# Kernel optimization log

Hardware: AMD Instinct MI355X
Metric: run time of the kernel (lower is better)

Reference implementation:

```python
import jax, jax.numpy as jnp
import numpy as np

H, D = 8, 16
HD = H * D
SCALE0 = float(1.0 / np.sqrt(D * 1))   # degree-0 dot-product scale (order m=1)
SCALE1 = float(1.0 / np.sqrt(D * 3))   # degree-1 dot-product scale (order m=3)
SHARED = float(np.sqrt(0.5))           # shared_scale = sqrt(1/2) for DOT_PROD + SHARED
NEG = -1e9


def _split_heads_q(x):  # (b,n,HD,m) -> (b,H,n,D,m)
    b, n, _, m = x.shape
    return x.reshape(b, n, H, D, m).transpose(0, 2, 1, 3, 4)


def _split_heads_k(x):  # (b,n,N,HD,m) -> (b,H,n,N,D,m)
    b, n, N, _, m = x.shape
    return x.reshape(b, n, N, H, D, m).transpose(0, 3, 1, 2, 4, 5)


def _augment_kv(k, v, feats, W_self, null_k, null_v):
    # attend_self: VNLinear self key/value; use_null_kv: learned null tokens.
    b, n = feats.shape[:2]
    m = feats.shape[-1]
    skv = jnp.einsum('oc,bncm->bnom', W_self, feats)          # (b,n,2HD,m)
    sk, sv = jnp.split(skv, 2, axis=-2)
    sk = _split_heads_q(sk)[:, :, :, None]                     # (b,H,n,1,D,m)
    sv = _split_heads_q(sv)[:, :, :, None]
    nk = jnp.broadcast_to(null_k[None, :, None, None], (b, H, n, 1, D, m))
    nv = jnp.broadcast_to(null_v[None, :, None, None], (b, H, n, 1, D, m))
    k = jnp.concatenate([nk, sk, k], axis=3)                   # (b,H,n,2+N,D,m)
    v = jnp.concatenate([nv, sv, v], axis=3)
    return k, v


def _merge_heads(x):  # (b,H,n,D,m) -> (b,n,HD,m)
    b, _, n, _, m = x.shape
    return x.transpose(0, 2, 1, 3, 4).reshape(b, n, HD, m)


def _forward(q0, k0, v0, q1, k1, v1, feats0, feats1, edges,
             W_self_kv0, W_self_kv1, W_bias, self_bias, null_bias,
             null_k0, null_v0, null_k1, null_v1, head_weights1,
             W_out0, W_out1, neighbor_mask):
    b, n, N = edges.shape[:3]
    q0h, k0h, v0h = _split_heads_q(q0), _split_heads_k(k0), _split_heads_k(v0)
    q1h, k1h, v1h = _split_heads_q(q1), _split_heads_k(k1), _split_heads_k(v1)
    k0h, v0h = _augment_kv(k0h, v0h, feats0, W_self_kv0, null_k0, null_v0)
    k1h, v1h = _augment_kv(k1h, v1h, feats1, W_self_kv1, null_k1, null_v1)

    # pair bias for degree 0 (to_order==1); prepend null/self bias columns
    edge_bias = jnp.einsum('bnje,he->bhnj', edges, W_bias)     # (b,H,n,N)
    nb = jnp.broadcast_to(null_bias[None, :, None, None], (b, H, n, 1))
    sb = jnp.broadcast_to(self_bias[None, :, None, None], (b, H, n, 1))
    bias = jnp.concatenate([nb, sb, edge_bias], axis=-1)        # (b,H,n,2+N)

    sim0 = jnp.einsum('bhndm,bhnjdm->bhnj', q0h, k0h) * SCALE0 + bias
    w1 = jax.nn.softplus(head_weights1)                         # (1,H,1,1)
    sim1 = jnp.einsum('bhndm,bhnjdm->bhnj', q1h, k1h) * (SCALE1 * w1)

    total = (sim0 + sim1) * SHARED
    mask = jnp.concatenate(
        [jnp.ones((b, 1, n, 2), dtype=bool),                    # null + self always valid
         neighbor_mask[:, None]], axis=-1)
    total = jnp.where(mask, total, NEG)
    attn = jax.nn.softmax(total, axis=-1)                       # shared across degrees

    out0 = _merge_heads(jnp.einsum('bhnj,bhnjdm->bhndm', attn, v0h))
    out1 = _merge_heads(jnp.einsum('bhnj,bhnjdm->bhndm', attn, v1h))

    y0 = jnp.einsum('oc,bncm->bnom', W_out0, out0)              # FiberLinear deg 0
    y1 = jnp.einsum('oc,bncm->bnom', W_out1, out1)              # FiberLinear deg 1
    return y0, y1


def setup_inputs() -> dict:
    key = jax.random.key(0)
    ks = jax.random.split(key, 20)
    b, n, N, e = 1, 2048, 32, 32
    d0, d1 = 128, 64
    f = lambda k, s: jax.random.normal(k, s, dtype=jnp.float32) * 0.1
    return {
        'q0': f(ks[0], (b, n, HD, 1)), 'k0': f(ks[1], (b, n, N, HD, 1)), 'v0': f(ks[2], (b, n, N, HD, 1)),
        'q1': f(ks[3], (b, n, HD, 3)), 'k1': f(ks[4], (b, n, N, HD, 3)), 'v1': f(ks[5], (b, n, N, HD, 3)),
        'feats0': f(ks[6], (b, n, d0, 1)), 'feats1': f(ks[7], (b, n, d1, 3)),
        'edges': f(ks[8], (b, n, N, e)),
        'W_self_kv0': f(ks[9], (2 * HD, d0)), 'W_self_kv1': f(ks[10], (2 * HD, d1)),
        'W_bias': f(ks[11], (H, e)),
        'self_bias': jnp.zeros((H,), jnp.float32), 'null_bias': jnp.zeros((H,), jnp.float32),
        'null_k0': jnp.zeros((H, D, 1), jnp.float32), 'null_v0': jnp.zeros((H, D, 1), jnp.float32),
        'null_k1': jnp.zeros((H, D, 3), jnp.float32), 'null_v1': jnp.zeros((H, D, 3), jnp.float32),
        'head_weights1': jnp.full((1, H, 1, 1), float(np.log(np.e - 1.0)), jnp.float32),
        'W_out0': f(ks[12], (d0, HD)), 'W_out1': f(ks[13], (d1, HD)),
        'neighbor_mask': jax.random.uniform(ks[14], (b, n, N)) > 0.1,
    }


def reference(q0, k0, v0, q1, k1, v1, feats0, feats1, edges,
              W_self_kv0, W_self_kv1, W_bias, self_bias, null_bias,
              null_k0, null_v0, null_k1, null_v1, head_weights1,
              W_out0, W_out1, neighbor_mask):
    return _forward(q0, k0, v0, q1, k1, v1, feats0, feats1, edges,
                    W_self_kv0, W_self_kv1, W_bias, self_bias, null_bias,
                    null_k0, null_v0, null_k1, null_v1, head_weights1,
                    W_out0, W_out1, neighbor_mask)
```

## Files before the change

kernel.cpp:

```cpp
#include <hip/hip_runtime.h>

constexpr int kH  = 8;
constexpr int kD  = 16;
constexpr int kHD = 128;
constexpr int kN  = 32;
constexpr int kE  = 32;
constexpr int kD0 = 128;
constexpr int kD1 = 64;
constexpr int kP  = 4;
constexpr int kP3 = 2;
constexpr int kPP = 8;

constexpr float SCALE0   = 0.25f;
constexpr float SCALE1   = 0.14433756729740643f;
constexpr float SHARED_S = 0.70710678118654752f;
constexpr float NEGV     = -1e9f;


__global__ __launch_bounds__(256) void k1_selfkv(
    const float* __restrict__ q0, const float* __restrict__ q1,
    const float* __restrict__ feats0, const float* __restrict__ feats1,
    const float* __restrict__ Wskv0, const float* __restrict__ Wskv1,
    const float* __restrict__ self_bias, const float* __restrict__ null_bias,
    const float* __restrict__ nk0, const float* __restrict__ nk1,
    const float* __restrict__ hw1,
    float* __restrict__ ws_sc, float* __restrict__ ws_sv0, float* __restrict__ ws_sv1)
{
  const int i0 = blockIdx.x * kP;
  const int t  = threadIdx.x;
  __shared__ __align__(16) float f0s[kP][kD0];
  __shared__ __align__(16) float f1s[kP][kD1 * 3];
  __shared__ __align__(16) float q0s[kP][kHD];
  __shared__ __align__(16) float q1s[kP][kHD * 3];
  __shared__ float sk0L[kP][kHD];
  __shared__ float sk1L[kP][kHD * 3];
  __shared__ float w1s[kH];

  for (int u = t; u < kP * 32; u += 256) { int p = u >> 5, r = u & 31;
    ((float4*)f0s[p])[r] = ((const float4*)(feats0 + (size_t)(i0 + p) * kD0))[r]; }
  for (int u = t; u < kP * 48; u += 256) { int p = u / 48, r = u % 48;
    ((float4*)f1s[p])[r] = ((const float4*)(feats1 + (size_t)(i0 + p) * kD1 * 3))[r]; }
  for (int u = t; u < kP * 32; u += 256) { int p = u >> 5, r = u & 31;
    ((float4*)q0s[p])[r] = ((const float4*)(q0 + (size_t)(i0 + p) * kHD))[r]; }
  for (int u = t; u < kP * 96; u += 256) { int p = u / 96, r = u % 96;
    ((float4*)q1s[p])[r] = ((const float4*)(q1 + (size_t)(i0 + p) * kHD * 3))[r]; }
  if (t < kH) w1s[t] = log1pf(expf(hw1[t]));
  __syncthreads();

  float acc0[kP] = {};
  {
    const float4* wr = (const float4*)(Wskv0 + t * kD0);
    #pragma unroll
    for (int g = 0; g < 32; ++g) {
      float4 w = wr[g]; int c = g * 4;
      #pragma unroll
      for (int p = 0; p < kP; ++p)
        acc0[p] += w.x * f0s[p][c] + w.y * f0s[p][c + 1]
                 + w.z * f0s[p][c + 2] + w.w * f0s[p][c + 3];
    }
  }
  float acc1[kP][3] = {};
  {
    const float4* wr = (const float4*)(Wskv1 + t * kD1);
    #pragma unroll
    for (int g = 0; g < 16; ++g) {
      float4 w = wr[g]; int c = g * 4;
      float wv[4] = {w.x, w.y, w.z, w.w};
      #pragma unroll
      for (int q = 0; q < 4; ++q) {
        #pragma unroll
        for (int p = 0; p < kP; ++p) {
          const float* fp = &f1s[p][(c + q) * 3];
          acc1[p][0] += wv[q] * fp[0];
          acc1[p][1] += wv[q] * fp[1];
          acc1[p][2] += wv[q] * fp[2];
        }
      }
    }
  }
  if (t < kHD) {
    #pragma unroll
    for (int p = 0; p < kP; ++p) {
      sk0L[p][t] = acc0[p];
      sk1L[p][t * 3 + 0] = acc1[p][0];
      sk1L[p][t * 3 + 1] = acc1[p][1];
      sk1L[p][t * 3 + 2] = acc1[p][2];
    }
  } else {
    const int o = t - kHD;
    #pragma unroll
    for (int p = 0; p < kP; ++p) {
      ws_sv0[(size_t)(i0 + p) * kHD + o] = acc0[p];
      float* sp = ws_sv1 + (size_t)(i0 + p) * kHD * 3 + o * 3;
      sp[0] = acc1[p][0]; sp[1] = acc1[p][1]; sp[2] = acc1[p][2];
    }
  }
  __syncthreads();

  if (t < kP * 16) {
    const int p = t >> 4, idx = t & 15;
    const int h = idx & 7;
    const bool is_self = idx >= 8;
    float s0 = 0.f, s1 = 0.f, bias;
    if (is_self) {
      #pragma unroll
      for (int d = 0; d < kD; ++d) s0 += q0s[p][h * kD + d] * sk0L[p][h * kD + d];
      #pragma unroll
      for (int x = 0; x < 48; ++x) s1 += q1s[p][h * 48 + x] * sk1L[p][h * 48 + x];
      bias = self_bias[h];
    } else {
      #pragma unroll
      for (int d = 0; d < kD; ++d) s0 += q0s[p][h * kD + d] * nk0[h * kD + d];
      #pragma unroll
      for (int x = 0; x < 48; ++x) s1 += q1s[p][h * 48 + x] * nk1[h * 48 + x];
      bias = null_bias[h];
    }
    float total = (s0 * SCALE0 + bias + s1 * SCALE1 * w1s[h]) * SHARED_S;
    ws_sc[(size_t)(i0 + p) * 272 + h * 34 + (is_self ? 1 : 0)] = total;
  }
}

__global__ __launch_bounds__(256) void k2_sims(
    const float* __restrict__ q0, const float* __restrict__ q1,
    const float* __restrict__ k0, const float* __restrict__ k1,
    const float* __restrict__ edges, const float* __restrict__ Wbias,
    const float* __restrict__ hw1, const int* __restrict__ nmask,
    float* __restrict__ ws_sc)
{
  const int i0 = blockIdx.x * kP;
  const int t  = threadIdx.x;
  __shared__ float q0s[kP][kH * 17];
  __shared__ float q1s[kP][kH * 49];
  __shared__ float edg[kP][kN * 33];
  __shared__ float wbT[kE * kH];
  __shared__ float w1s[kH];
  __shared__ __align__(16) float scL[kP][272];

  for (int u = t; u < kP * 32; u += 256) { int p = u >> 5, r = u & 31;
    float4 v = ((const float4*)(q0 + (size_t)(i0 + p) * kHD))[r];
    int c = r * 4, h = c >> 4, d = c & 15;
    float* dst = &q0s[p][h * 17 + d];
    dst[0] = v.x; dst[1] = v.y; dst[2] = v.z; dst[3] = v.w; }
  for (int u = t; u < kP * 96; u += 256) { int p = u / 96, r = u % 96;
    float4 v = ((const float4*)(q1 + (size_t)(i0 + p) * kHD * 3))[r];
    int c = r * 4, h = c / 48, x = c % 48;
    float* dst = &q1s[p][h * 49 + x];
    dst[0] = v.x; dst[1] = v.y; dst[2] = v.z; dst[3] = v.w; }
  for (int u = t; u < kP * 256; u += 256) { int p = u >> 8, r = u & 255;
    float4 v = ((const float4*)(edges + (size_t)(i0 + p) * kN * kE))[r];
    int j = r >> 3, e4 = (r & 7) * 4;
    float* dst = &edg[p][j * 33 + e4];
    dst[0] = v.x; dst[1] = v.y; dst[2] = v.z; dst[3] = v.w; }
  if (t < kH * kE) { int h = t >> 5, e = t & 31; wbT[e * 8 + h] = Wbias[t]; }
  if (t < kH) w1s[t] = log1pf(expf(hw1[t]));
  if (t < kP * 16) { int p = t >> 4, idx = t & 15, h = idx & 7, slot = idx >> 3;
    scL[p][h * 34 + slot] = ws_sc[(size_t)(i0 + p) * 272 + h * 34 + slot]; }
  __syncthreads();

  {
    const int j = t >> 3, h = t & 7;
    #pragma unroll
    for (int p = 0; p < kP; ++p) {
      const int i = i0 + p;
      float bias = 0.f;
      #pragma unroll
      for (int e = 0; e < kE; ++e) bias += edg[p][j * 33 + e] * wbT[e * 8 + h];
      float s0 = 0.f;
      const float4* kr0 = (const float4*)(k0 + (size_t)(i * kN + j) * kHD + h * kD);
      #pragma unroll
      for (int g = 0; g < 4; ++g) {
        float4 w = kr0[g]; int x = h * 17 + g * 4;
        s0 += w.x * q0s[p][x] + w.y * q0s[p][x + 1]
            + w.z * q0s[p][x + 2] + w.w * q0s[p][x + 3];
      }
      float s1 = 0.f;
      const float4* kr1 = (const float4*)(k1 + (size_t)(i * kN + j) * kHD * 3 + h * 48);
      #pragma unroll
      for (int g = 0; g < 12; ++g) {
        float4 w = kr1[g]; int x = h * 49 + g * 4;
        s1 += w.x * q1s[p][x] + w.y * q1s[p][x + 1]
            + w.z * q1s[p][x + 2] + w.w * q1s[p][x + 3];
      }
      float total = (s0 * SCALE0 + bias + s1 * SCALE1 * w1s[h]) * SHARED_S;
      bool valid = nmask[(size_t)i * kN + j] != 0;
      scL[p][h * 34 + 2 + j] = valid ? total : NEGV;
    }
  }
  __syncthreads();

  if (t < kP * kH) {
    const int p = t >> 3, h = t & 7;
    float* row = &scL[p][h * 34];
    float mx = -1e30f;
    #pragma unroll
    for (int u = 0; u < 34; ++u) mx = fmaxf(mx, row[u]);
    float sum = 0.f;
    #pragma unroll
    for (int u = 0; u < 34; ++u) sum += __expf(row[u] - mx);
    float inv = 1.f / sum;
    #pragma unroll
    for (int u = 0; u < 34; ++u) row[u] = __expf(row[u] - mx) * inv;
  }
  __syncthreads();

  for (int u = t; u < kP * 68; u += 256) {
    int p = u / 68, r = u % 68;
    ((float4*)(ws_sc + (size_t)(i0 + p) * 272))[r] = ((float4*)scL[p])[r];
  }
}

__global__ __launch_bounds__(256, 4) void k3_accum(
    const float* __restrict__ v0, const float* __restrict__ v1,
    const float* __restrict__ nv0, const float* __restrict__ nv1,
    const float* __restrict__ ws_sc,
    float* __restrict__ ws_sv0, float* __restrict__ ws_sv1)
{
  const int i0 = blockIdx.x * kP3;
  const int t  = threadIdx.x;
  __shared__ __align__(16) float attnL[kP3][272];

  if (t < kP3 * 68) {
    int p = t / 68, r = t % 68;
    ((float4*)attnL[p])[r] = ((const float4*)(ws_sc + (size_t)(i0 + p) * 272))[r];
  }
  __syncthreads();

  const int p = t >> 7, i = i0 + p;
  const int s = t & 127;
  float4 acc;
  if (s < 32) {
    const int h = s >> 2;
    const float* at = attnL[p] + h * 34;
    float4 nv = ((const float4*)nv0)[s];
    float4 sv = ((const float4*)(ws_sv0 + (size_t)i * kHD))[s];
    acc.x = at[0] * nv.x + at[1] * sv.x;
    acc.y = at[0] * nv.y + at[1] * sv.y;
    acc.z = at[0] * nv.z + at[1] * sv.z;
    acc.w = at[0] * nv.w + at[1] * sv.w;
    const float4* vp = (const float4*)(v0 + (size_t)i * kN * kHD) + s;
    float4 vbuf[8];
    #pragma unroll
    for (int g = 0; g < 4; ++g) {
      #pragma unroll
      for (int r = 0; r < 8; ++r) vbuf[r] = vp[(g * 8 + r) * 32];
      #pragma unroll
      for (int r = 0; r < 8; ++r) {
        float a = at[2 + g * 8 + r];
        acc.x += a * vbuf[r].x; acc.y += a * vbuf[r].y;
        acc.z += a * vbuf[r].z; acc.w += a * vbuf[r].w;
      }
    }
    ((float4*)(ws_sv0 + (size_t)i * kHD))[s] = acc;
  } else {
    const int s1 = s - 32;
    const int h = s1 / 12;
    const float* at = attnL[p] + h * 34;
    float4 nv = ((const float4*)nv1)[s1];
    float4 sv = ((const float4*)(ws_sv1 + (size_t)i * kHD * 3))[s1];
    acc.x = at[0] * nv.x + at[1] * sv.x;
    acc.y = at[0] * nv.y + at[1] * sv.y;
    acc.z = at[0] * nv.z + at[1] * sv.z;
    acc.w = at[0] * nv.w + at[1] * sv.w;
    const float4* vp = (const float4*)(v1 + (size_t)i * kN * kHD * 3) + s1;
    float4 vbuf[8];
    #pragma unroll
    for (int g = 0; g < 4; ++g) {
      #pragma unroll
      for (int r = 0; r < 8; ++r) vbuf[r] = vp[(g * 8 + r) * 96];
      #pragma unroll
      for (int r = 0; r < 8; ++r) {
        float a = at[2 + g * 8 + r];
        acc.x += a * vbuf[r].x; acc.y += a * vbuf[r].y;
        acc.z += a * vbuf[r].z; acc.w += a * vbuf[r].w;
      }
    }
    ((float4*)(ws_sv1 + (size_t)i * kHD * 3))[s1] = acc;
  }
}

__global__ __launch_bounds__(320) void k4_proj(
    const float* __restrict__ ws_o0, const float* __restrict__ ws_o1,
    const float* __restrict__ Wout0, const float* __restrict__ Wout1,
    float* __restrict__ out, int n_total)
{
  const int i0 = blockIdx.x * kPP;
  const int t  = threadIdx.x;
  __shared__ __align__(16) float o0L[kPP][kHD];
  __shared__ __align__(16) float o1L[kPP][kHD * 3];

  for (int u = t; u < kPP * 32; u += 320) { int p = u >> 5, r = u & 31;
    ((float4*)o0L[p])[r] = ((const float4*)(ws_o0 + (size_t)(i0 + p) * kHD))[r]; }
  for (int u = t; u < kPP * 96; u += 320) { int p = u / 96, r = u % 96;
    ((float4*)o1L[p])[r] = ((const float4*)(ws_o1 + (size_t)(i0 + p) * kHD * 3))[r]; }
  __syncthreads();

  if (t < 128) {
    float acc[kPP] = {};
    const float4* wr = (const float4*)(Wout0 + t * kHD);
    #pragma unroll
    for (int g = 0; g < 32; ++g) {
      float4 w = wr[g]; int c = g * 4;
      #pragma unroll
      for (int p = 0; p < kPP; ++p)
        acc[p] += w.x * o0L[p][c] + w.y * o0L[p][c + 1]
                + w.z * o0L[p][c + 2] + w.w * o0L[p][c + 3];
    }
    #pragma unroll
    for (int p = 0; p < kPP; ++p) out[(size_t)(i0 + p) * kHD + t] = acc[p];
  } else {
    const int v2 = t - 128, o = v2 / 3, m = v2 - o * 3;
    float acc[kPP] = {};
    const float4* wr = (const float4*)(Wout1 + o * kHD);
    #pragma unroll
    for (int g = 0; g < 32; ++g) {
      float4 w = wr[g]; int c = g * 4;
      #pragma unroll
      for (int p = 0; p < kPP; ++p)
        acc[p] += w.x * o1L[p][(c + 0) * 3 + m] + w.y * o1L[p][(c + 1) * 3 + m]
                + w.z * o1L[p][(c + 2) * 3 + m] + w.w * o1L[p][(c + 3) * 3 + m];
    }
    #pragma unroll
    for (int p = 0; p < kPP; ++p)
      out[(size_t)n_total * kHD + (size_t)(i0 + p) * 192 + v2] = acc[p];
  }
}

extern "C" void kernel_launch(void* const* d_in, const int* in_sizes, int n_in,
                              void* d_out, int out_size, void* d_ws, size_t ws_size,
                              hipStream_t stream) {
  const int n = in_sizes[0] / kHD;
  const float* q0     = (const float*)d_in[0];
  const float* k0     = (const float*)d_in[1];
  const float* v0     = (const float*)d_in[2];
  const float* q1     = (const float*)d_in[3];
  const float* k1     = (const float*)d_in[4];
  const float* v1     = (const float*)d_in[5];
  const float* feats0 = (const float*)d_in[6];
  const float* feats1 = (const float*)d_in[7];
  const float* edges  = (const float*)d_in[8];
  const float* Wskv0  = (const float*)d_in[9];
  const float* Wskv1  = (const float*)d_in[10];
  const float* Wbias  = (const float*)d_in[11];
  const float* sbias  = (const float*)d_in[12];
  const float* nbias  = (const float*)d_in[13];
  const float* nk0    = (const float*)d_in[14];
  const float* nv0    = (const float*)d_in[15];
  const float* nk1    = (const float*)d_in[16];
  const float* nv1    = (const float*)d_in[17];
  const float* hw1    = (const float*)d_in[18];
  const float* Wout0  = (const float*)d_in[19];
  const float* Wout1  = (const float*)d_in[20];
  const int*   nmask  = (const int*)d_in[21];

  float* ws     = (float*)d_ws;
  float* ws_sc  = ws;
  float* ws_sv0 = ws + (size_t)n * 272;
  float* ws_sv1 = ws + (size_t)n * 272 + (size_t)n * 128;

  k1_selfkv<<<n / kP, 256, 0, stream>>>(q0, q1, feats0, feats1, Wskv0, Wskv1,
                                        sbias, nbias, nk0, nk1, hw1,
                                        ws_sc, ws_sv0, ws_sv1);
  k2_sims<<<n / kP, 256, 0, stream>>>(q0, q1, k0, k1, edges, Wbias, hw1, nmask, ws_sc);
  k3_accum<<<n / kP3, 256, 0, stream>>>(v0, v1, nv0, nv1, ws_sc, ws_sv0, ws_sv1);
  k4_proj<<<n / kPP, 320, 0, stream>>>(ws_sv0, ws_sv1, Wout0, Wout1, (float*)d_out, n);
}
```

Baseline: 360.5 us.

## Process one node per block in k2 and do softmax with warp shuffles

The similarity kernel now launches one block per query node instead of four. Each thread handles a single (head, neighbor) pair, with threads mapped so that a head's 32 neighbors fall in consecutive lanes. The shared-memory softmax pass, done serially by a few threads, is replaced by shuffle-xor reductions for max and sum, and results are written straight to the workspace, removing two block barriers. This trades more blocks and reloading of the shared Wbias/hw1 per node for better parallelism in the softmax. Because the 32-lane shuffle reductions sit inside a 64-wide wavefront, the correctness of the reduction depends on the xor offsets staying within 32-lane groups.

```diff
diff --git a/kernel.cpp b/kernel.cpp
--- a/kernel.cpp
+++ b/kernel.cpp
@@ -127,86 +127,72 @@
     const float* __restrict__ hw1, const int* __restrict__ nmask,
     float* __restrict__ ws_sc)
 {
-  const int i0 = blockIdx.x * kP;
-  const int t  = threadIdx.x;
-  __shared__ float q0s[kP][kH * 17];
-  __shared__ float q1s[kP][kH * 49];
-  __shared__ float edg[kP][kN * 33];
-  __shared__ float wbT[kE * kH];
+  const int i = blockIdx.x;
+  const int t = threadIdx.x;
+  __shared__ __align__(16) float q0s[kHD];
+  __shared__ __align__(16) float q1s[kHD * 3];
+  __shared__ __align__(16) float edg[kN][kE + 1];
+  __shared__ float wbs[kH * kE];
   __shared__ float w1s[kH];
-  __shared__ __align__(16) float scL[kP][272];
-
-  for (int u = t; u < kP * 32; u += 256) { int p = u >> 5, r = u & 31;
-    float4 v = ((const float4*)(q0 + (size_t)(i0 + p) * kHD))[r];
-    int c = r * 4, h = c >> 4, d = c & 15;
-    float* dst = &q0s[p][h * 17 + d];
-    dst[0] = v.x; dst[1] = v.y; dst[2] = v.z; dst[3] = v.w; }
-  for (int u = t; u < kP * 96; u += 256) { int p = u / 96, r = u % 96;
-    float4 v = ((const float4*)(q1 + (size_t)(i0 + p) * kHD * 3))[r];
-    int c = r * 4, h = c / 48, x = c % 48;
-    float* dst = &q1s[p][h * 49 + x];
-    dst[0] = v.x; dst[1] = v.y; dst[2] = v.z; dst[3] = v.w; }
-  for (int u = t; u < kP * 256; u += 256) { int p = u >> 8, r = u & 255;
-    float4 v = ((const float4*)(edges + (size_t)(i0 + p) * kN * kE))[r];
-    int j = r >> 3, e4 = (r & 7) * 4;
-    float* dst = &edg[p][j * 33 + e4];
-    dst[0] = v.x; dst[1] = v.y; dst[2] = v.z; dst[3] = v.w; }
-  if (t < kH * kE) { int h = t >> 5, e = t & 31; wbT[e * 8 + h] = Wbias[t]; }
+
+  if (t < 32) {
+    ((float4*)q0s)[t] = ((const float4*)(q0 + (size_t)i * kHD))[t];
+  } else if (t < 128) {
+    int r = t - 32;
+    ((float4*)q1s)[r] = ((const float4*)(q1 + (size_t)i * kHD * 3))[r];
+  }
+  {
+    float4 v = ((const float4*)(edges + (size_t)i * kN * kE))[t];
+    int j = t >> 3, e4 = (t & 7) * 4;
+    float* dst = &edg[j][e4];
+    dst[0] = v.x; dst[1] = v.y; dst[2] = v.z; dst[3] = v.w;
+  }
+  if (t < kH * kE) wbs[t] = Wbias[t];
   if (t < kH) w1s[t] = log1pf(expf(hw1[t]));
-  if (t < kP * 16) { int p = t >> 4, idx = t & 15, h = idx & 7, slot = idx >> 3;
-    scL[p][h * 34 + slot] = ws_sc[(size_t)(i0 + p) * 272 + h * 34 + slot]; }
-  __syncthreads();
-
-  {
-    const int j = t >> 3, h = t & 7;
-    #pragma unroll
-    for (int p = 0; p < kP; ++p) {
-      const int i = i0 + p;
-      float bias = 0.f;
-      #pragma unroll
-      for (int e = 0; e < kE; ++e) bias += edg[p][j * 33 + e] * wbT[e * 8 + h];
-      float s0 = 0.f;
-      const float4* kr0 = (const float4*)(k0 + (size_t)(i * kN + j) * kHD + h * kD);
-      #pragma unroll
-      for (int g = 0; g < 4; ++g) {
-        float4 w = kr0[g]; int x = h * 17 + g * 4;
-        s0 += w.x * q0s[p][x] + w.y * q0s[p][x + 1]
-            + w.z * q0s[p][x + 2] + w.w * q0s[p][x + 3];
-      }
-      float s1 = 0.f;
-      const float4* kr1 = (const float4*)(k1 + (size_t)(i * kN + j) * kHD * 3 + h * 48);
-      #pragma unroll
-      for (int g = 0; g < 12; ++g) {
-        float4 w = kr1[g]; int x = h * 49 + g * 4;
-        s1 += w.x * q1s[p][x] + w.y * q1s[p][x + 1]
-            + w.z * q1s[p][x + 2] + w.w * q1s[p][x + 3];
-      }
-      float total = (s0 * SCALE0 + bias + s1 * SCALE1 * w1s[h]) * SHARED_S;
-      bool valid = nmask[(size_t)i * kN + j] != 0;
-      scL[p][h * 34 + 2 + j] = valid ? total : NEGV;
-    }
-  }
-  __syncthreads();
-
-  if (t < kP * kH) {
-    const int p = t >> 3, h = t & 7;
-    float* row = &scL[p][h * 34];
-    float mx = -1e30f;
-    #pragma unroll
-    for (int u = 0; u < 34; ++u) mx = fmaxf(mx, row[u]);
-    float sum = 0.f;
-    #pragma unroll
-    for (int u = 0; u < 34; ++u) sum += __expf(row[u] - mx);
-    float inv = 1.f / sum;
-    #pragma unroll
-    for (int u = 0; u < 34; ++u) row[u] = __expf(row[u] - mx) * inv;
-  }
-  __syncthreads();
-
-  for (int u = t; u < kP * 68; u += 256) {
-    int p = u / 68, r = u % 68;
-    ((float4*)(ws_sc + (size_t)(i0 + p) * 272))[r] = ((float4*)scL[p])[r];
-  }
+  __syncthreads();
+
+  const int h = t >> 5, j = t & 31;
+
+  float bias = 0.f;
+  #pragma unroll
+  for (int e = 0; e < kE; ++e) bias += edg[j][e] * wbs[h * kE + e];
+
+  float s0 = 0.f;
+  const float4* kr0 = (const float4*)(k0 + ((size_t)i * kN + j) * kHD + h * kD);
+  #pragma unroll
+  for (int g = 0; g < 4; ++g) {
+    float4 w = kr0[g]; int x = h * kD + g * 4;
+    s0 += w.x * q0s[x] + w.y * q0s[x + 1] + w.z * q0s[x + 2] + w.w * q0s[x + 3];
+  }
+  float s1 = 0.f;
+  const float4* kr1 = (const float4*)(k1 + ((size_t)i * kN + j) * kHD * 3 + h * 48);
+  #pragma unroll
+  for (int g = 0; g < 12; ++g) {
+    float4 w = kr1[g]; int x = h * 48 + g * 4;
+    s1 += w.x * q1s[x] + w.y * q1s[x + 1] + w.z * q1s[x + 2] + w.w * q1s[x + 3];
+  }
+
+  float total = (s0 * SCALE0 + bias + s1 * SCALE1 * w1s[h]) * SHARED_S;
+  bool valid = nmask[(size_t)i * kN + j] != 0;
+  float sc = valid ? total : NEGV;
+
+  float* row = ws_sc + (size_t)i * 272 + h * 34;
+  float e0v = row[0], e1v = row[1];
+
+  float mx = sc;
+  #pragma unroll
+  for (int off = 16; off > 0; off >>= 1) mx = fmaxf(mx, __shfl_xor(mx, off));
+  mx = fmaxf(mx, fmaxf(e0v, e1v));
+  float ex = __expf(sc - mx);
+  float sum = ex;
+  #pragma unroll
+  for (int off = 16; off > 0; off >>= 1) sum += __shfl_xor(sum, off);
+  float ee0 = __expf(e0v - mx), ee1 = __expf(e1v - mx);
+  float inv = 1.f / (sum + ee0 + ee1);
+
+  row[2 + j] = ex * inv;
+  if (j == 0) row[0] = ee0 * inv;
+  if (j == 1) row[1] = ee1 * inv;
 }
 
 __global__ __launch_bounds__(256, 4) void k3_accum(
@@ -360,7 +346,7 @@
   k1_selfkv<<<n / kP, 256, 0, stream>>>(q0, q1, feats0, feats1, Wskv0, Wskv1,
                                         sbias, nbias, nk0, nk1, hw1,
                                         ws_sc, ws_sv0, ws_sv1);
-  k2_sims<<<n / kP, 256, 0, stream>>>(q0, q1, k0, k1, edges, Wbias, hw1, nmask, ws_sc);
+  k2_sims<<<n, 256, 0, stream>>>(q0, q1, k0, k1, edges, Wbias, hw1, nmask, ws_sc);
   k3_accum<<<n / kP3, 256, 0, stream>>>(v0, v1, nv0, nv1, ws_sc, ws_sv0, ws_sv1);
   k4_proj<<<n / kPP, 320, 0, stream>>>(ws_sv0, ws_sv1, Wout0, Wout1, (float*)d_out, n);
 }
```

New measurement: 364.0 us. About the same (+1.0%).
